# Kernel optimization log

Measured on AMD Instinct MI355X. Metric: run time of the kernel, lower is better.

## Reference

```python
import jax, jax.numpy as jnp
import numpy as np

B, CIN, C, H, W = 2, 64, 32, 64, 64

def conv3(x, w, b):
    # 3x3 conv, stride 1, SAME padding, followed by ReLU (matches conv(..., relu=True))
    y = jax.lax.conv_general_dilated(x, w, (1, 1), 'SAME',
                                     dimension_numbers=('NCHW', 'OIHW', 'NCHW'))
    return jax.nn.relu(y + b[None, :, None, None])

def setup_inputs() -> dict:
    key = jax.random.key(0)
    ks = jax.random.split(key, 24)
    def wgt(k, o, i):
        return jax.random.normal(k, (o, i, 3, 3), dtype=jnp.float32) * 0.05
    def bias(o):
        return jnp.zeros((o,), dtype=jnp.float32)
    return {
        'x':   jax.random.normal(ks[0], (B, CIN, H, W), dtype=jnp.float32),
        'wq1': wgt(ks[1], C, CIN), 'bq1': bias(C), 'wq2': wgt(ks[2], C, C), 'bq2': bias(C),
        'wk1': wgt(ks[3], C, CIN), 'bk1': bias(C), 'wk2': wgt(ks[4], C, C), 'bk2': bias(C),
        'wv1': wgt(ks[5], C, CIN), 'bv1': bias(C), 'wv2': wgt(ks[6], C, C), 'bv2': bias(C),
        'wr': wgt(ks[7], C, C),  'br': bias(C),
        'wg': wgt(ks[8], C, C),  'bg': bias(C),
        'wb': wgt(ks[9], C, C),  'bb': bias(C),
        'w2': wgt(ks[10], C, CIN + C), 'b2': bias(C),
        'w3': wgt(ks[11], C, C), 'b3': bias(C),
    }

def reference(x, wq1, bq1, wq2, bq2, wk1, bk1, wk2, bk2, wv1, bv1, wv2, bv2,
              wr, br, wg, bg, wb, bb, w2, b2, w3, b3):
    b, c, h, w = x.shape
    scale = C ** (-0.5)
    # query/key/value projections: two stacked 3x3 conv+relu each
    q = conv3(conv3(x, wq1, bq1), wq2, bq2).reshape(b, C, h * w)  # [b,C,N]
    k = conv3(conv3(x, wk1, bk1), wk2, bk2).reshape(b, C, h * w)
    v = conv3(conv3(x, wv1, bv1), wv2, bv2).reshape(b, C, h * w)
    qT = jnp.swapaxes(q, 1, 2)  # [b,N,C]
    vT = jnp.swapaxes(v, 1, 2)  # [b,N,C]
    # pass 1: softmax(Q^T K) V^T
    sim1 = jax.nn.softmax(scale * jnp.einsum('bnc,bcm->bnm', qT, k), axis=-1)
    ctx1 = jnp.einsum('bnm,bmc->bnc', sim1, vT)  # [b,N,C]
    ctx1 = conv3(jnp.swapaxes(ctx1, 1, 2).reshape(b, C, h, w), wr, br)
    # pass 2: softmax(K^T V) Q^T
    sim2 = jax.nn.softmax(scale * jnp.einsum('bnc,bcm->bnm', jnp.swapaxes(k, 1, 2), v), axis=-1)
    ctx2 = jnp.einsum('bnm,bmc->bnc', sim2, qT)
    ctx2 = conv3(jnp.swapaxes(ctx2, 1, 2).reshape(b, C, h, w), wg, bg)
    # pass 3: softmax(V^T Q) K^T
    sim3 = jax.nn.softmax(scale * jnp.einsum('bnc,bcm->bnm', vT, q), axis=-1)
    ctx3 = jnp.einsum('bnm,bmc->bnc', sim3, jnp.swapaxes(k, 1, 2))
    ctx3 = conv3(jnp.swapaxes(ctx3, 1, 2).reshape(b, C, h, w), wb, bb)
    ctx = (ctx1 + ctx2 + ctx3) / 3.0
    out = conv3(jnp.concatenate([x, ctx], axis=1), w2, b2)
    out = conv3(out, w3, b3)
    return out
```

## Files before the change

### kernel.cpp

```cpp
#include <hip/hip_runtime.h>
#include <hip/hip_bf16.h>
#include <math.h>

#define N_PIX 4096
#define CCH 32
#define BB 2
#define PIX_P 4356

typedef __attribute__((ext_vector_type(8))) short short8;
typedef __attribute__((ext_vector_type(4))) float f32x4;
typedef __attribute__((ext_vector_type(16))) float f32x16;

struct PrepPar {
  __hip_bfloat16* bz[16]; int bzsch[16];
  const float* wsrc[11];
  const float* x;
  __hip_bfloat16* xcat;
  __hip_bfloat16* wbf;
};

__global__ __launch_bounds__(256) void prep_k(PrepPar p)
{
  const int blk = blockIdx.x, t = threadIdx.x;
  if (blk < 16) {
    const int sch = p.bzsch[blk];
    __hip_bfloat16* __restrict__ ptr = p.bz[blk];
    const int total = 260*sch;
    for (int j = t; j < total; j += 256) {
      int e = j / sch, c = j - e*sch;
      int yy, xx;
      if (e < 66)       { yy = 0;       xx = e; }
      else if (e < 132) { yy = 65;      xx = e - 66; }
      else if (e < 196) { yy = e - 131; xx = 0; }
      else              { yy = e - 195; xx = 65; }
      ptr[((size_t)yy*66 + xx)*sch + c] = __float2bfloat16(0.f);
    }
  } else if (blk < 80) {
    const int csum[12] = {0,18432,36864,55296,64512,73728,82944,92160,
                          101376,110592,138240,147456};
    const int wcin[11] = {64,64,64,32,32,32,32,32,32,96,32};
    for (int j = (blk-16)*256 + t; j < 147456; j += 64*256) {
      int s = 0;
      #pragma unroll
      for (int q = 1; q <= 10; ++q) s += (j >= csum[q]);
      const int jj = j - csum[s];
      const int cin = wcin[s], K = 9*cin;
      const int co = jj / K, k = jj - co*K;
      const int kk = k / cin, ci = k - kk*cin;
      p.wbf[j] = __float2bfloat16(p.wsrc[s][(size_t)(co*cin + ci)*9 + kk]);
    }
  } else {
    const int b2 = blk - 80;
    const int y = b2 & 63, b = b2 >> 6;
    for (int j = t; j < 4096; j += 256) {
      int ci = j >> 6, xx = j & 63;
      float v = p.x[((size_t)(b*64 + ci)*64 + y)*64 + xx];
      p.xcat[((size_t)b*PIX_P + (size_t)(y+1)*66 + xx+1)*96 + ci] = __float2bfloat16(v);
    }
  }
}

struct ConvPar {
  const __hip_bfloat16* in[3];
  const __hip_bfloat16* wb[3];
  const float* bias[3];
  __hip_bfloat16* outPad[3];
  __hip_bfloat16* outPix[3];
  __hip_bfloat16* outCh[3];
  float* outF[3];
  int mode, sch;
};

template<int CIN>
__global__ __launch_bounds__(256) void conv_mfma(ConvPar p)
{
  constexpr int K = 9*CIN;
  constexpr int S = K/32;
  constexpr int Q = S/4, R = S%4;
  constexpr int e0 = Q + (R>0 ? 1:0);
  constexpr int e1 = e0 + Q + (R>1 ? 1:0);
  constexpr int e2 = e1 + Q + (R>2 ? 1:0);
  const int sel = blockIdx.y, b = blockIdx.z;
  const int sch = p.sch;
  const __hip_bfloat16* __restrict__ in = p.in[sel] + (size_t)b*PIX_P*sch;
  const __hip_bfloat16* __restrict__ wb = p.wb[sel];
  const float* __restrict__ bias = p.bias[sel];
  const int t = threadIdx.x, wave = t >> 6, lane = t & 63;
  const int l15 = lane & 15, q4 = lane >> 4;
  const int y = blockIdx.x >> 2;
  const int xw = (blockIdx.x & 3)*16;

  __shared__ float red[3][16][33];

  f32x4 acc0 = {0.f,0.f,0.f,0.f}, acc1 = {0.f,0.f,0.f,0.f};

#define CONV_BODY(ks)                                                          \
  {                                                                            \
    const int kk  = ((ks)*32)/CIN;                                             \
    const int ci0 = ((ks)*32)%CIN + q4*8;                                      \
    const int dy = kk/3 - 1, dx = (kk%3) - 1;                                  \
    const short8 bw0 = *(const short8*)&wb[(size_t)l15*K      + (ks)*32 + q4*8]; \
    const short8 bw1 = *(const short8*)&wb[(size_t)(16+l15)*K + (ks)*32 + q4*8]; \
    const short8 av  = *(const short8*)&in[((size_t)(y+1+dy)*66 + xw + l15 + 1 + dx)*sch + ci0]; \
    acc0 = __builtin_amdgcn_mfma_f32_16x16x32_bf16(av, bw0, acc0, 0, 0, 0);    \
    acc1 = __builtin_amdgcn_mfma_f32_16x16x32_bf16(av, bw1, acc1, 0, 0, 0);    \
  }

  if (wave == 0) {
    #pragma unroll
    for (int ks = 0; ks < e0; ++ks) CONV_BODY(ks)
  } else if (wave == 1) {
    #pragma unroll
    for (int ks = e0; ks < e1; ++ks) CONV_BODY(ks)
  } else if (wave == 2) {
    #pragma unroll
    for (int ks = e1; ks < e2; ++ks) CONV_BODY(ks)
  } else {
    #pragma unroll
    for (int ks = e2; ks < S; ++ks) CONV_BODY(ks)
  }
#undef CONV_BODY

  if (wave > 0) {
    #pragma unroll
    for (int r = 0; r < 4; ++r) {
      red[wave-1][q4*4 + r][l15]      = acc0[r];
      red[wave-1][q4*4 + r][16 + l15] = acc1[r];
    }
  }
  __syncthreads();
  if (wave == 0) {
    const float bz0 = bias[l15], bz1 = bias[16 + l15];
    #pragma unroll
    for (int r = 0; r < 4; ++r) {
      const int px = q4*4 + r;
      const float v0 = fmaxf(acc0[r] + red[0][px][l15] + red[1][px][l15]
                             + red[2][px][l15] + bz0, 0.f);
      const float v1 = fmaxf(acc1[r] + red[0][px][16+l15] + red[1][px][16+l15]
                             + red[2][px][16+l15] + bz1, 0.f);
      const int xx = xw + px;
      const int pix = y*64 + xx;
      if (p.mode & 1) {
        __hip_bfloat16* o = p.outPad[sel] + ((size_t)b*PIX_P + (size_t)(y+1)*66 + xx+1)*32;
        o[l15] = __float2bfloat16(v0); o[16+l15] = __float2bfloat16(v1);
      }
      if (p.mode & 2) {
        __hip_bfloat16* o = p.outPix[sel] + ((size_t)b*N_PIX + pix)*32;
        o[l15] = __float2bfloat16(v0); o[16+l15] = __float2bfloat16(v1);
      }
      if (p.mode & 4) {
        __hip_bfloat16* o = p.outCh[sel] + (size_t)b*32*N_PIX
                            + (size_t)(pix >> 5)*1024 + (pix & 31);
        o[(size_t)l15*32]      = __float2bfloat16(v0);
        o[(size_t)(16+l15)*32] = __float2bfloat16(v1);
      }
      if (p.mode & 8) {
        float* o = p.outF[sel] + (size_t)b*32*N_PIX + pix;
        o[(size_t)l15*N_PIX]      = v0;
        o[(size_t)(16+l15)*N_PIX] = v1;
      }
    }
  }
}

struct A3Par {
  const __hip_bfloat16* ctxP;
  const __hip_bfloat16* wb[3];
  const float* bias[3];
  __hip_bfloat16* xcat;
};

__global__ __launch_bounds__(192) void a3avg_k(A3Par p)
{
  constexpr int K = 288;
  const int t = threadIdx.x, wave = t >> 6, lane = t & 63;
  const int l15 = lane & 15, q4 = lane >> 4;
  const int b = blockIdx.y;
  const int y = blockIdx.x >> 2;
  const int xw = (blockIdx.x & 3)*16;
  const int sel = wave;
  const __hip_bfloat16* __restrict__ in = p.ctxP + ((size_t)(sel*BB + b))*PIX_P*32;
  const __hip_bfloat16* __restrict__ wb = p.wb[sel];
  const float* __restrict__ bias = p.bias[sel];

  __shared__ float red[2][16][33];

  f32x4 acc0 = {0.f,0.f,0.f,0.f}, acc1 = {0.f,0.f,0.f,0.f};
  #pragma unroll
  for (int ks = 0; ks < 9; ++ks) {
    const int dy = ks/3 - 1, dx = (ks%3) - 1;
    const short8 bw0 = *(const short8*)&wb[(size_t)l15*K      + ks*32 + q4*8];
    const short8 bw1 = *(const short8*)&wb[(size_t)(16+l15)*K + ks*32 + q4*8];
    const short8 av  = *(const short8*)&in[((size_t)(y+1+dy)*66 + xw + l15 + 1 + dx)*32 + q4*8];
    acc0 = __builtin_amdgcn_mfma_f32_16x16x32_bf16(av, bw0, acc0, 0, 0, 0);
    acc1 = __builtin_amdgcn_mfma_f32_16x16x32_bf16(av, bw1, acc1, 0, 0, 0);
  }
  const float bz0 = bias[l15], bz1 = bias[16 + l15];
  #pragma unroll
  for (int r = 0; r < 4; ++r) {
    acc0[r] = fmaxf(acc0[r] + bz0, 0.f);
    acc1[r] = fmaxf(acc1[r] + bz1, 0.f);
  }
  if (wave > 0) {
    #pragma unroll
    for (int r = 0; r < 4; ++r) {
      red[wave-1][q4*4 + r][l15]      = acc0[r];
      red[wave-1][q4*4 + r][16 + l15] = acc1[r];
    }
  }
  __syncthreads();
  if (wave == 0) {
    #pragma unroll
    for (int r = 0; r < 4; ++r) {
      const int px = q4*4 + r;
      const float v0 = (acc0[r] + red[0][px][l15]    + red[1][px][l15])    * (1.0f/3.0f);
      const float v1 = (acc1[r] + red[0][px][16+l15] + red[1][px][16+l15]) * (1.0f/3.0f);
      const int xx = xw + px;
      __hip_bfloat16* o = p.xcat + ((size_t)b*PIX_P + (size_t)(y+1)*66 + xx+1)*96 + 64;
      o[l15]      = __float2bfloat16(v0);
      o[16 + l15] = __float2bfloat16(v1);
    }
  }
}

__global__ __launch_bounds__(512, 6) void attn_mfma(
    const __hip_bfloat16* __restrict__ qP, const __hip_bfloat16* __restrict__ kP,
    const __hip_bfloat16* __restrict__ vP,
    const __hip_bfloat16* __restrict__ qT, const __hip_bfloat16* __restrict__ kT,
    const __hip_bfloat16* __restrict__ vT,
    __hip_bfloat16* __restrict__ ctxPad)
{
  const int pass = blockIdx.y, b = blockIdx.z;
  const __hip_bfloat16 *XT, *YT, *ZT;
  if (pass == 0)      { XT = qP; YT = kP; ZT = vT; }
  else if (pass == 1) { XT = kP; YT = vP; ZT = qT; }
  else                { XT = vP; YT = qP; ZT = kT; }
  const size_t boff = (size_t)b * CCH * N_PIX;
  XT += boff; YT += boff; ZT += boff;
  __hip_bfloat16* __restrict__ ctx = ctxPad + ((size_t)(pass*BB + b))*PIX_P*32;

  const int t = threadIdx.x;
  const int wave = t >> 6, lane = t & 63;
  const int l31 = lane & 31, l5 = lane >> 5;
  const int n0 = blockIdx.x * 32;
  const int mbase = wave * (N_PIX/8);

  __shared__ float mgO[7][16][64];
  __shared__ float mgD[8][32];

  const short8 bx0 = *(const short8*)&XT[(size_t)(n0 + l31)*CCH + l5*8];
  const short8 bx1 = *(const short8*)&XT[(size_t)(n0 + l31)*CCH + 16 + l5*8];

  f32x16 oacc = {0,0,0,0,0,0,0,0,0,0,0,0,0,0,0,0};
  float rs0 = 0.f, rs1 = 0.f, rs2 = 0.f, rs3 = 0.f;
  const float SC2 = 0.17677669529663687f * 1.4426950408889634f;
  const float OFF = 20.0f;

  #pragma unroll 2
  for (int m0 = mbase; m0 < mbase + N_PIX/8; m0 += 32) {
    const short8 ay0 = *(const short8*)&YT[(size_t)(m0 + l31)*CCH + l5*8];
    const short8 ay1 = *(const short8*)&YT[(size_t)(m0 + l31)*CCH + 16 + l5*8];
    f32x16 s = {0,0,0,0,0,0,0,0,0,0,0,0,0,0,0,0};
    s = __builtin_amdgcn_mfma_f32_32x32x16_bf16(ay0, bx0, s, 0, 0, 0);
    s = __builtin_amdgcn_mfma_f32_32x32x16_bf16(ay1, bx1, s, 0, 0, 0);

    float p[16];
    #pragma unroll
    for (int r = 0; r < 16; ++r) {
      const float arg = fmaf(s[r], SC2, -OFF);
      asm("v_exp_f32 %0, %1" : "=v"(p[r]) : "v"(arg));
    }
    #pragma unroll
    for (int r = 0; r < 4; ++r) {
      rs0 += p[r];
      rs1 += p[4 + r];
      rs2 += p[8 + r];
      rs3 += p[12 + r];
    }

    unsigned w[8];
    #pragma unroll
    for (int h = 0; h < 8; ++h) {
      const int rhi = h >> 1, j = h & 1;
      asm("v_cvt_pk_bf16_f32 %0, %1, %2"
          : "=v"(w[h]) : "v"(p[rhi*4 + 2*j]), "v"(p[rhi*4 + 2*j + 1]));
    }
    asm("v_permlane32_swap_b32 %0, %1" : "+v"(w[2]), "+v"(w[0]));
    asm("v_permlane32_swap_b32 %0, %1" : "+v"(w[3]), "+v"(w[1]));
    asm("v_permlane32_swap_b32 %0, %1" : "+v"(w[6]), "+v"(w[4]));
    asm("v_permlane32_swap_b32 %0, %1" : "+v"(w[7]), "+v"(w[5]));
    union U { unsigned u[4]; short8 v8; };
    U A0, A1;
    A0.u[0] = w[0]; A0.u[1] = w[1]; A0.u[2] = w[2]; A0.u[3] = w[3];
    A1.u[0] = w[4]; A1.u[1] = w[5]; A1.u[2] = w[6]; A1.u[3] = w[7];

    const short8 bz0 = *(const short8*)&ZT[(size_t)(m0 + l31)*32 + l5*8];
    const short8 bz1 = *(const short8*)&ZT[(size_t)(m0 + l31)*32 + 16 + l5*8];
    oacc = __builtin_amdgcn_mfma_f32_32x32x16_bf16(A0.v8, bz0, oacc, 0, 0, 0);
    oacc = __builtin_amdgcn_mfma_f32_32x32x16_bf16(A1.v8, bz1, oacc, 0, 0, 0);
  }

  float rs = (rs0 + rs1) + (rs2 + rs3);
  rs += __shfl_xor(rs, 32);
  if (l5 == 0) mgD[wave][l31] = rs;
  if (wave) {
    #pragma unroll
    for (int r = 0; r < 16; ++r) mgO[wave-1][r][lane] = oacc[r];
  }
  __syncthreads();
  if (wave == 0) {
    #pragma unroll
    for (int r = 0; r < 16; ++r) {
      const int i = (r & 3) + 8*(r >> 2) + 4*l5;
      float den = 0.f, tot = oacc[r];
      #pragma unroll
      for (int ww = 0; ww < 8; ++ww) den += mgD[ww][i];
      #pragma unroll
      for (int ww = 0; ww < 7; ++ww) tot += mgO[ww][r][lane];
      const int pix = n0 + i;
      const int yy = pix >> 6, xx = pix & 63;
      ctx[((size_t)(yy+1)*66 + xx+1)*32 + l31] = __float2bfloat16(tot / den);
    }
  }
}

extern "C" void kernel_launch(void* const* d_in, const int* in_sizes, int n_in,
                              void* d_out, int out_size, void* d_ws, size_t ws_size,
                              hipStream_t stream)
{
  const float* x   = (const float*)d_in[0];
  const float* wq1 = (const float*)d_in[1];  const float* bq1 = (const float*)d_in[2];
  const float* wq2 = (const float*)d_in[3];  const float* bq2 = (const float*)d_in[4];
  const float* wk1 = (const float*)d_in[5];  const float* bk1 = (const float*)d_in[6];
  const float* wk2 = (const float*)d_in[7];  const float* bk2 = (const float*)d_in[8];
  const float* wv1 = (const float*)d_in[9];  const float* bv1 = (const float*)d_in[10];
  const float* wv2 = (const float*)d_in[11]; const float* bv2 = (const float*)d_in[12];
  const float* wr  = (const float*)d_in[13]; const float* br  = (const float*)d_in[14];
  const float* wg  = (const float*)d_in[15]; const float* bg  = (const float*)d_in[16];
  const float* wb_ = (const float*)d_in[17]; const float* bb_ = (const float*)d_in[18];
  const float* w2  = (const float*)d_in[19]; const float* b2  = (const float*)d_in[20];
  const float* w3  = (const float*)d_in[21]; const float* b3  = (const float*)d_in[22];

  char* base = (char*)d_ws;
  __hip_bfloat16* xcat  = (__hip_bfloat16*)(base + 0);
  __hip_bfloat16* q1p   = (__hip_bfloat16*)(base + 1672704);
  __hip_bfloat16* ctxP  = (__hip_bfloat16*)(base + 3345408);
  __hip_bfloat16* out4p = (__hip_bfloat16*)(base + 5018112);
  __hip_bfloat16* qkvP  = (__hip_bfloat16*)(base + 5575680);
  __hip_bfloat16* qkvT  = (__hip_bfloat16*)(base + 7148544);
  __hip_bfloat16* wbf   = (__hip_bfloat16*)(base + 8721408);
  const size_t PADSLOT = (size_t)BB*PIX_P*32;
  const size_t UPSLOT  = (size_t)BB*N_PIX*32;

  PrepPar pp;
  for (int i = 0; i < 2; ++i)  { pp.bz[i]    = xcat  + (size_t)i*PIX_P*96; pp.bzsch[i]    = 96; }
  for (int i = 0; i < 6; ++i)  { pp.bz[2+i]  = q1p   + (size_t)i*PIX_P*32; pp.bzsch[2+i]  = 32; }
  for (int i = 0; i < 6; ++i)  { pp.bz[8+i]  = ctxP  + (size_t)i*PIX_P*32; pp.bzsch[8+i]  = 32; }
  for (int i = 0; i < 2; ++i)  { pp.bz[14+i] = out4p + (size_t)i*PIX_P*32; pp.bzsch[14+i] = 32; }
  const float* wsrc[11] = {wq1,wk1,wv1,wq2,wk2,wv2,wr,wg,wb_,w2,w3};
  for (int i = 0; i < 11; ++i) pp.wsrc[i] = wsrc[i];
  pp.x = x; pp.xcat = xcat; pp.wbf = wbf;
  prep_k<<<dim3(208), dim3(256), 0, stream>>>(pp);

  ConvPar c1 = {};
  for (int i = 0; i < 3; ++i) c1.in[i] = xcat;
  c1.wb[0]=wbf+0; c1.wb[1]=wbf+18432; c1.wb[2]=wbf+36864;
  c1.bias[0]=bq1; c1.bias[1]=bk1; c1.bias[2]=bv1;
  c1.outPad[0]=q1p; c1.outPad[1]=q1p+PADSLOT; c1.outPad[2]=q1p+2*PADSLOT;
  c1.mode = 1; c1.sch = 96;
  conv_mfma<64><<<dim3(256, 3, BB), dim3(256), 0, stream>>>(c1);

  ConvPar c2 = {};
  c2.in[0]=q1p; c2.in[1]=q1p+PADSLOT; c2.in[2]=q1p+2*PADSLOT;
  c2.wb[0]=wbf+55296; c2.wb[1]=wbf+64512; c2.wb[2]=wbf+73728;
  c2.bias[0]=bq2; c2.bias[1]=bk2; c2.bias[2]=bv2;
  c2.outPix[0]=qkvP; c2.outPix[1]=qkvP+UPSLOT; c2.outPix[2]=qkvP+2*UPSLOT;
  c2.outCh[0]=qkvT;  c2.outCh[1]=qkvT+UPSLOT;  c2.outCh[2]=qkvT+2*UPSLOT;
  c2.mode = 6; c2.sch = 32;
  conv_mfma<32><<<dim3(256, 3, BB), dim3(256), 0, stream>>>(c2);

  attn_mfma<<<dim3(N_PIX/32, 3, BB), dim3(512), 0, stream>>>(
      qkvP, qkvP+UPSLOT, qkvP+2*UPSLOT, qkvT, qkvT+UPSLOT, qkvT+2*UPSLOT, ctxP);

  A3Par a3;
  a3.ctxP = ctxP;
  a3.wb[0]=wbf+82944; a3.wb[1]=wbf+92160; a3.wb[2]=wbf+101376;
  a3.bias[0]=br; a3.bias[1]=bg; a3.bias[2]=bb_;
  a3.xcat = xcat;
  a3avg_k<<<dim3(256, BB), dim3(192), 0, stream>>>(a3);

  ConvPar c4 = {};
  c4.in[0]=xcat; c4.wb[0]=wbf+110592; c4.bias[0]=b2;
  c4.outPad[0]=out4p; c4.mode = 1; c4.sch = 96;
  conv_mfma<96><<<dim3(256, 1, BB), dim3(256), 0, stream>>>(c4);

  ConvPar c5 = {};
  c5.in[0]=out4p; c5.wb[0]=wbf+138240; c5.bias[0]=b3;
  c5.outF[0]=(float*)d_out; c5.mode = 8; c5.sch = 32;
  conv_mfma<32><<<dim3(256, 1, BB), dim3(256), 0, stream>>>(c5);
}
```

Measured before the change: 73.88 us.

## Process two 32-row query tiles per attention block to reuse key/value loads

Each attention block now handles 64 query pixels as two 32-row groups, so each Y (key) and Z (value) tile loaded in the inner loop feeds two sets of MFMA/softmax work. This halves the global loads of Y/Z per query and halves the grid size. In exchange it needs more registers (two accumulators) and doubles the shared-memory reduction buffers, and the occupancy hint drops from 6 to 4 blocks, leaving fewer blocks (384) to fill the GPU.

Measured after the change: 78.38 us. 6.1% more time.

```diff
diff --git a/kernel.cpp b/kernel.cpp
--- a/kernel.cpp
+++ b/kernel.cpp
@@ -223,7 +223,7 @@
   }
 }
 
-__global__ __launch_bounds__(512, 6) void attn_mfma(
+__global__ __launch_bounds__(512, 4) void attn_mfma(
     const __hip_bfloat16* __restrict__ qP, const __hip_bfloat16* __restrict__ kP,
     const __hip_bfloat16* __restrict__ vP,
     const __hip_bfloat16* __restrict__ qT, const __hip_bfloat16* __restrict__ kT,
@@ -242,84 +242,99 @@
   const int t = threadIdx.x;
   const int wave = t >> 6, lane = t & 63;
   const int l31 = lane & 31, l5 = lane >> 5;
-  const int n0 = blockIdx.x * 32;
+  const int n0 = blockIdx.x * 64;
   const int mbase = wave * (N_PIX/8);
 
-  __shared__ float mgO[7][16][64];
-  __shared__ float mgD[8][32];
-
-  const short8 bx0 = *(const short8*)&XT[(size_t)(n0 + l31)*CCH + l5*8];
-  const short8 bx1 = *(const short8*)&XT[(size_t)(n0 + l31)*CCH + 16 + l5*8];
-
-  f32x16 oacc = {0,0,0,0,0,0,0,0,0,0,0,0,0,0,0,0};
-  float rs0 = 0.f, rs1 = 0.f, rs2 = 0.f, rs3 = 0.f;
+  __shared__ float mgO[2][7][16][64];
+  __shared__ float mgD[2][8][32];
+
+  const short8 bxA0 = *(const short8*)&XT[(size_t)(n0 + l31)*CCH + l5*8];
+  const short8 bxA1 = *(const short8*)&XT[(size_t)(n0 + l31)*CCH + 16 + l5*8];
+  const short8 bxB0 = *(const short8*)&XT[(size_t)(n0 + 32 + l31)*CCH + l5*8];
+  const short8 bxB1 = *(const short8*)&XT[(size_t)(n0 + 32 + l31)*CCH + 16 + l5*8];
+
+  f32x16 oaccA = {0,0,0,0,0,0,0,0,0,0,0,0,0,0,0,0};
+  f32x16 oaccB = {0,0,0,0,0,0,0,0,0,0,0,0,0,0,0,0};
+  float rsA0 = 0.f, rsA1 = 0.f, rsB0 = 0.f, rsB1 = 0.f;
   const float SC2 = 0.17677669529663687f * 1.4426950408889634f;
   const float OFF = 20.0f;
 
-  #pragma unroll 2
   for (int m0 = mbase; m0 < mbase + N_PIX/8; m0 += 32) {
     const short8 ay0 = *(const short8*)&YT[(size_t)(m0 + l31)*CCH + l5*8];
     const short8 ay1 = *(const short8*)&YT[(size_t)(m0 + l31)*CCH + 16 + l5*8];
-    f32x16 s = {0,0,0,0,0,0,0,0,0,0,0,0,0,0,0,0};
-    s = __builtin_amdgcn_mfma_f32_32x32x16_bf16(ay0, bx0, s, 0, 0, 0);
-    s = __builtin_amdgcn_mfma_f32_32x32x16_bf16(ay1, bx1, s, 0, 0, 0);
-
-    float p[16];
-    #pragma unroll
-    for (int r = 0; r < 16; ++r) {
-      const float arg = fmaf(s[r], SC2, -OFF);
-      asm("v_exp_f32 %0, %1" : "=v"(p[r]) : "v"(arg));
-    }
-    #pragma unroll
-    for (int r = 0; r < 4; ++r) {
-      rs0 += p[r];
-      rs1 += p[4 + r];
-      rs2 += p[8 + r];
-      rs3 += p[12 + r];
-    }
-
-    unsigned w[8];
-    #pragma unroll
-    for (int h = 0; h < 8; ++h) {
-      const int rhi = h >> 1, j = h & 1;
-      asm("v_cvt_pk_bf16_f32 %0, %1, %2"
-          : "=v"(w[h]) : "v"(p[rhi*4 + 2*j]), "v"(p[rhi*4 + 2*j + 1]));
-    }
-    asm("v_permlane32_swap_b32 %0, %1" : "+v"(w[2]), "+v"(w[0]));
-    asm("v_permlane32_swap_b32 %0, %1" : "+v"(w[3]), "+v"(w[1]));
-    asm("v_permlane32_swap_b32 %0, %1" : "+v"(w[6]), "+v"(w[4]));
-    asm("v_permlane32_swap_b32 %0, %1" : "+v"(w[7]), "+v"(w[5]));
-    union U { unsigned u[4]; short8 v8; };
-    U A0, A1;
-    A0.u[0] = w[0]; A0.u[1] = w[1]; A0.u[2] = w[2]; A0.u[3] = w[3];
-    A1.u[0] = w[4]; A1.u[1] = w[5]; A1.u[2] = w[6]; A1.u[3] = w[7];
-
     const short8 bz0 = *(const short8*)&ZT[(size_t)(m0 + l31)*32 + l5*8];
     const short8 bz1 = *(const short8*)&ZT[(size_t)(m0 + l31)*32 + 16 + l5*8];
-    oacc = __builtin_amdgcn_mfma_f32_32x32x16_bf16(A0.v8, bz0, oacc, 0, 0, 0);
-    oacc = __builtin_amdgcn_mfma_f32_32x32x16_bf16(A1.v8, bz1, oacc, 0, 0, 0);
-  }
-
-  float rs = (rs0 + rs1) + (rs2 + rs3);
-  rs += __shfl_xor(rs, 32);
-  if (l5 == 0) mgD[wave][l31] = rs;
+
+#define QGROUP(bxg0, bxg1, oaccg, rsg0, rsg1)                                  \
+    {                                                                          \
+      f32x16 s = {0,0,0,0,0,0,0,0,0,0,0,0,0,0,0,0};                            \
+      s = __builtin_amdgcn_mfma_f32_32x32x16_bf16(ay0, bxg0, s, 0, 0, 0);      \
+      s = __builtin_amdgcn_mfma_f32_32x32x16_bf16(ay1, bxg1, s, 0, 0, 0);      \
+      float p[16];                                                             \
+      _Pragma("unroll")                                                        \
+      for (int r = 0; r < 16; ++r) {                                           \
+        const float arg = fmaf(s[r], SC2, -OFF);                               \
+        asm("v_exp_f32 %0, %1" : "=v"(p[r]) : "v"(arg));                       \
+      }                                                                        \
+      _Pragma("unroll")                                                        \
+      for (int r = 0; r < 8; ++r) { rsg0 += p[r]; rsg1 += p[8 + r]; }          \
+      unsigned w[8];                                                           \
+      _Pragma("unroll")                                                        \
+      for (int h = 0; h < 8; ++h) {                                            \
+        const int rhi = h >> 1, j = h & 1;                                     \
+        asm("v_cvt_pk_bf16_f32 %0, %1, %2"                                     \
+            : "=v"(w[h]) : "v"(p[rhi*4 + 2*j]), "v"(p[rhi*4 + 2*j + 1]));      \
+      }                                                                        \
+      asm("v_permlane32_swap_b32 %0, %1" : "+v"(w[2]), "+v"(w[0]));            \
+      asm("v_permlane32_swap_b32 %0, %1" : "+v"(w[3]), "+v"(w[1]));            \
+      asm("v_permlane32_swap_b32 %0, %1" : "+v"(w[6]), "+v"(w[4]));            \
+      asm("v_permlane32_swap_b32 %0, %1" : "+v"(w[7]), "+v"(w[5]));            \
+      union U { unsigned u[4]; short8 v8; };                                   \
+      U A0, A1;                                                                \
+      A0.u[0] = w[0]; A0.u[1] = w[1]; A0.u[2] = w[2]; A0.u[3] = w[3];          \
+      A1.u[0] = w[4]; A1.u[1] = w[5]; A1.u[2] = w[6]; A1.u[3] = w[7];          \
+      oaccg = __builtin_amdgcn_mfma_f32_32x32x16_bf16(A0.v8, bz0, oaccg, 0, 0, 0); \
+      oaccg = __builtin_amdgcn_mfma_f32_32x32x16_bf16(A1.v8, bz1, oaccg, 0, 0, 0); \
+    }
+
+    QGROUP(bxA0, bxA1, oaccA, rsA0, rsA1)
+    QGROUP(bxB0, bxB1, oaccB, rsB0, rsB1)
+#undef QGROUP
+  }
+
+  float rsA = rsA0 + rsA1;
+  float rsB = rsB0 + rsB1;
+  rsA += __shfl_xor(rsA, 32);
+  rsB += __shfl_xor(rsB, 32);
+  if (l5 == 0) { mgD[0][wave][l31] = rsA; mgD[1][wave][l31] = rsB; }
   if (wave) {
     #pragma unroll
-    for (int r = 0; r < 16; ++r) mgO[wave-1][r][lane] = oacc[r];
+    for (int r = 0; r < 16; ++r) {
+      mgO[0][wave-1][r][lane] = oaccA[r];
+      mgO[1][wave-1][r][lane] = oaccB[r];
+    }
   }
   __syncthreads();
   if (wave == 0) {
     #pragma unroll
     for (int r = 0; r < 16; ++r) {
       const int i = (r & 3) + 8*(r >> 2) + 4*l5;
-      float den = 0.f, tot = oacc[r];
+      float denA = 0.f, totA = oaccA[r];
+      float denB = 0.f, totB = oaccB[r];
       #pragma unroll
-      for (int ww = 0; ww < 8; ++ww) den += mgD[ww][i];
+      for (int ww = 0; ww < 8; ++ww) { denA += mgD[0][ww][i]; denB += mgD[1][ww][i]; }
       #pragma unroll
-      for (int ww = 0; ww < 7; ++ww) tot += mgO[ww][r][lane];
-      const int pix = n0 + i;
-      const int yy = pix >> 6, xx = pix & 63;
-      ctx[((size_t)(yy+1)*66 + xx+1)*32 + l31] = __float2bfloat16(tot / den);
+      for (int ww = 0; ww < 7; ++ww) { totA += mgO[0][ww][r][lane]; totB += mgO[1][ww][r][lane]; }
+      {
+        const int pix = n0 + i;
+        const int yy = pix >> 6, xx = pix & 63;
+        ctx[((size_t)(yy+1)*66 + xx+1)*32 + l31] = __float2bfloat16(totA / denA);
+      }
+      {
+        const int pix = n0 + 32 + i;
+        const int yy = pix >> 6, xx = pix & 63;
+        ctx[((size_t)(yy+1)*66 + xx+1)*32 + l31] = __float2bfloat16(totB / denB);
+      }
     }
   }
 }
@@ -379,7 +394,7 @@
   c2.mode = 6; c2.sch = 32;
   conv_mfma<32><<<dim3(256, 3, BB), dim3(256), 0, stream>>>(c2);
 
-  attn_mfma<<<dim3(N_PIX/32, 3, BB), dim3(512), 0, stream>>>(
+  attn_mfma<<<dim3(N_PIX/64, 3, BB), dim3(512), 0, stream>>>(
       qkvP, qkvP+UPSLOT, qkvP+2*UPSLOT, qkvT, qkvT+UPSLOT, qkvT+2*UPSLOT, ctxP);
 
   A3Par a3;
```
